# Optimization experiments

Measured on AMD Instinct MI355X. Metric: run time of the kernel, lower is better.

The kernel has to match this reference:

```python
import jax, jax.numpy as jnp
import numpy as np

B, T, NEMBD, HEAD = 8, 2048, 1024, 64

def setup_inputs() -> dict:
    key = jax.random.key(0)
    ks = jax.random.split(key, 6)
    return {
        "values": jax.random.normal(ks[0], (B, T, NEMBD), dtype=jnp.float32),
        "keys": jax.random.normal(ks[1], (B, T, NEMBD), dtype=jnp.float32),
        "queries": jax.random.normal(ks[2], (B, T, NEMBD), dtype=jnp.float32),
        "Wk": jax.random.normal(ks[3], (NEMBD, HEAD), dtype=jnp.float32) * (NEMBD ** -0.5),
        "Wq": jax.random.normal(ks[4], (NEMBD, HEAD), dtype=jnp.float32) * (NEMBD ** -0.5),
        "Wv": jax.random.normal(ks[5], (NEMBD, HEAD), dtype=jnp.float32) * (NEMBD ** -0.5),
    }

def reference(values, keys, queries, Wk, Wq, Wv):
    Bq, Tq, C = queries.shape  # C = nEmbd; original scales by C**-0.5 (NOT headSize)
    k = keys @ Wk              # [B,T,H]
    q = queries @ Wq           # [B,T,H]
    v = values @ Wv            # [B,T,H]
    weight = jnp.einsum('bth,bsh->bts', q, k) * (C ** -0.5)  # [B,T,T]
    causal = jnp.tril(jnp.ones((Tq, Tq), dtype=bool))
    weight = jnp.where(causal, weight, -jnp.inf)
    weight = jax.nn.softmax(weight, axis=-1)
    # dropout = 0.0 (eval): identity
    out = jnp.einsum('bts,bsh->bth', weight, v)  # [B,T,H]
    return out
```

## Files before the change

kernel.cpp:

```cpp
#include <hip/hip_runtime.h>
#include <hip/hip_bf16.h>

typedef __bf16 bf16x8 __attribute__((ext_vector_type(8)));
typedef float f32x4 __attribute__((ext_vector_type(4)));
typedef unsigned short u16x8 __attribute__((ext_vector_type(8)));

#define NB 8
#define NT 2048
#define NC 1024
#define NH 64

__device__ __forceinline__ unsigned short bfbits(float f) {
    return __builtin_bit_cast(unsigned short, (__bf16)f);
}

__device__ __forceinline__ void gl_lds16(const void* g, void* l) {
    __builtin_amdgcn_global_load_lds(
        (const __attribute__((address_space(1))) void*)g,
        (__attribute__((address_space(3))) void*)l, 16, 0, 0);
}
__device__ __forceinline__ void gl_lds16_nt(const void* g, void* l) {
    __builtin_amdgcn_global_load_lds(
        (const __attribute__((address_space(1))) void*)g,
        (__attribute__((address_space(3))) void*)l, 16, 0, 2);
}

__global__ __launch_bounds__(256) void wt_kernel(const float* __restrict__ Wq,
                                                 const float* __restrict__ Wk,
                                                 const float* __restrict__ Wv,
                                                 unsigned short* __restrict__ Wt) {
    int idx = blockIdx.x * 256 + threadIdx.x;
    int n = idx >> 16;
    int r = idx & 65535;
    int c = r >> 6;
    int h = r & 63;
    const float* W = (n == 0) ? Wq : ((n == 1) ? Wk : Wv);
    float x = W[c * 64 + h];
    Wt[(n << 16) + h * 1024 + c] = bfbits(x);
}

__global__ __launch_bounds__(256, 3) void proj_kernel(const float* __restrict__ Xv,
                                                      const float* __restrict__ Xk,
                                                      const float* __restrict__ Xq,
                                                      const unsigned short* __restrict__ Wt,
                                                      unsigned short* __restrict__ Q,
                                                      unsigned short* __restrict__ K,
                                                      unsigned short* __restrict__ VT) {
    __shared__ __align__(16) char Xs[2][16384];
    __shared__ __align__(16) char Ws[2][8192];

    int type = blockIdx.x >> 8;
    int mt   = blockIdx.x & 255;
    int row0 = mt << 6;
    int phase = mt & 15;
    const float* X = (type == 0) ? Xq : ((type == 1) ? Xk : Xv);

    int tid  = threadIdx.x;
    int w    = tid >> 6;
    int lane = tid & 63;
    int lo = lane & 15, hi = lane >> 4;
    int swz = (lo & 7) << 4;

    const char* Xbase = (const char*)X + (size_t)row0 * 4096;
    const char* Wbase = (const char*)(Wt + (type << 16));

    int xr_l = lane >> 4;
    int xc_l = (lane & 15) * 16;
    int wr_l = lane >> 3;
    int wc_l = (lane & 7) * 16;

    f32x4 acc[4];
#pragma unroll
    for (int ct = 0; ct < 4; ++ct) acc[ct] = 0.f;

    auto stage = [&](int kc, int buf) {
#pragma unroll
        for (int i = 0; i < 4; ++i) {
            int g = w * 4 + i;
            int r = g * 4 + xr_l;
            gl_lds16_nt(Xbase + (size_t)r * 4096 + kc * 256 + (xc_l ^ ((r & 7) << 4)),
                        Xs[buf] + g * 1024);
        }
#pragma unroll
        for (int i = 0; i < 2; ++i) {
            int g = w * 2 + i;
            int h = g * 8 + wr_l;
            gl_lds16(Wbase + (size_t)h * 2048 + kc * 128 + (wc_l ^ ((h & 7) << 4)),
                     Ws[buf] + g * 1024);
        }
    };

    auto compute = [&](int buf) {
        const char* xrow = Xs[buf] + (w * 16 + lo) * 256;
        const char* wb   = Ws[buf];
#pragma unroll
        for (int ks = 0; ks < 2; ++ks) {
            f32x4 a0 = *(const f32x4*)(xrow + ((ks * 128 + hi * 32) ^ swz));
            f32x4 a1 = *(const f32x4*)(xrow + ((ks * 128 + hi * 32 + 16) ^ swz));
            bf16x8 af;
            af[0] = (__bf16)a0[0]; af[1] = (__bf16)a0[1]; af[2] = (__bf16)a0[2]; af[3] = (__bf16)a0[3];
            af[4] = (__bf16)a1[0]; af[5] = (__bf16)a1[1]; af[6] = (__bf16)a1[2]; af[7] = (__bf16)a1[3];
#pragma unroll
            for (int ct = 0; ct < 4; ++ct) {
                bf16x8 bf = *(const bf16x8*)(wb + (ct * 16 + lo) * 128 + ((ks * 64 + hi * 16) ^ swz));
                acc[ct] = __builtin_amdgcn_mfma_f32_16x16x32_bf16(af, bf, acc[ct], 0, 0, 0);
            }
        }
    };

    stage(phase, 0);
    stage((1 + phase) & 15, 1);

    for (int c = 0; c < 16; ++c) {
        int buf = c & 1;
        if (c < 15) asm volatile("s_waitcnt vmcnt(6)" ::: "memory");
        else        asm volatile("s_waitcnt vmcnt(0)" ::: "memory");
        __builtin_amdgcn_s_barrier();
        compute(buf);
        if (c + 2 < 16) {
            __builtin_amdgcn_s_barrier();
            stage((c + 2 + phase) & 15, buf);
        }
    }

    if (type < 2) {
        unsigned short* O = (type == 0) ? Q : K;
#pragma unroll
        for (int ct = 0; ct < 4; ++ct)
#pragma unroll
            for (int r = 0; r < 4; ++r) {
                int row = row0 + w * 16 + hi * 4 + r;
                int h = lo + 16 * ct;
                O[(size_t)row * NH + h] = bfbits(acc[ct][r]);
            }
    } else {
        int trow = row0 + w * 16 + hi * 4;
        int b = trow >> 11;
        int t = trow & 2047;
#pragma unroll
        for (int ct = 0; ct < 4; ++ct) {
            int h = lo + 16 * ct;
            ushort4 pk;
            pk.x = bfbits(acc[ct][0]);
            pk.y = bfbits(acc[ct][1]);
            pk.z = bfbits(acc[ct][2]);
            pk.w = bfbits(acc[ct][3]);
            *(ushort4*)(VT + (size_t)(b * NH + h) * NT + t) = pk;
        }
    }
}

__global__ __launch_bounds__(256, 2) void attn_kernel(const unsigned short* __restrict__ Q,
                                                      const unsigned short* __restrict__ K,
                                                      const unsigned short* __restrict__ VT,
                                                      float* __restrict__ out) {
    __shared__ __align__(16) unsigned short p_lds[4 * 1024];
    __shared__ __align__(16) float acc_lds[4 * 16 * 64];
    __shared__ float l_lds[4][16];

    int b = blockIdx.x & 7;
    int j = blockIdx.x >> 3;
    int w    = threadIdx.x >> 6;
    int lane = threadIdx.x & 63;
    int lo = lane & 15, hi = lane >> 4;

    const float SC = 0.03125f * 1.44269504088896340736f;
    unsigned short* pl = p_lds + w * 1024;
    char* plb = (char*)pl;

    for (int t2 = 0; t2 < 2; ++t2) {
        int qt = t2 ? (127 - j) : j;
        int q0 = qt << 4;

        const unsigned short* qb = Q + (size_t)(b * NT + q0 + lo) * NH + hi * 8;
        bf16x8 qr0 = *(const bf16x8*)(qb);
        bf16x8 qr1 = *(const bf16x8*)(qb + 32);
        bf16x8 qf0, qf1;
#pragma unroll
        for (int jj = 0; jj < 8; ++jj) {
            qf0[jj] = (__bf16)((float)qr0[jj] * SC);
            qf1[jj] = (__bf16)((float)qr1[jj] * SC);
        }

        int Ct = (q0 + 79) >> 6;
        int c0 = (Ct * w) >> 2;
        int c1 = (Ct * (w + 1)) >> 2;

        float l[4];
        f32x4 acc[4];
#pragma unroll
        for (int r = 0; r < 4; ++r) l[r] = 0.f;
#pragma unroll
        for (int ct = 0; ct < 4; ++ct) acc[ct] = 0.f;

        bf16x8 kn[8], vn[8];
        if (c0 < c1) {
            const unsigned short* kp = K + (size_t)(b * NT + (c0 << 6) + lo) * NH + hi * 8;
            const unsigned short* vp = VT + (size_t)(b * NH + lo) * NT + (c0 << 6) + hi * 8;
#pragma unroll
            for (int g = 0; g < 4; ++g) {
                kn[2 * g]     = *(const bf16x8*)(kp + g * 16 * NH);
                kn[2 * g + 1] = *(const bf16x8*)(kp + g * 16 * NH + 32);
                vn[2 * g]     = *(const bf16x8*)(vp + g * 16 * NT);
                vn[2 * g + 1] = *(const bf16x8*)(vp + g * 16 * NT + 32);
            }
        }

        for (int c = c0; c < c1; ++c) {
            int s0 = c << 6;
            bf16x8 kk[8], vv[8];
#pragma unroll
            for (int i = 0; i < 8; ++i) { kk[i] = kn[i]; vv[i] = vn[i]; }
            if (c + 1 < c1) {
                const unsigned short* kp2 = K + (size_t)(b * NT + ((c + 1) << 6) + lo) * NH + hi * 8;
                const unsigned short* vp2 = VT + (size_t)(b * NH + lo) * NT + ((c + 1) << 6) + hi * 8;
#pragma unroll
                for (int g = 0; g < 4; ++g) {
                    kn[2 * g]     = *(const bf16x8*)(kp2 + g * 16 * NH);
                    kn[2 * g + 1] = *(const bf16x8*)(kp2 + g * 16 * NH + 32);
                    vn[2 * g]     = *(const bf16x8*)(vp2 + g * 16 * NT);
                    vn[2 * g + 1] = *(const bf16x8*)(vp2 + g * 16 * NT + 32);
                }
            }

            f32x4 S[4];
#pragma unroll
            for (int t = 0; t < 4; ++t) {
                f32x4 s = 0.f;
                s = __builtin_amdgcn_mfma_f32_16x16x32_bf16(qf0, kk[2 * t], s, 0, 0, 0);
                s = __builtin_amdgcn_mfma_f32_16x16x32_bf16(qf1, kk[2 * t + 1], s, 0, 0, 0);
                S[t] = s;
            }

#pragma unroll
            for (int r = 0; r < 4; ++r) {
                int qi = q0 + hi * 4 + r;
                int ql = hi * 4 + r;
                int sw = (ql & 7) << 4;
                float psum = 0.f;
#pragma unroll
                for (int t = 0; t < 4; ++t) {
                    int sk = s0 + t * 16 + lo;
                    float p = (sk <= qi) ? exp2f(S[t][r] - 32.f) : 0.f;
                    psum += p;
                    int byte = ql * 128 + ((((t * 16 + lo) * 2)) ^ sw);
                    *(unsigned short*)(plb + byte) = bfbits(p);
                }
                l[r] += psum;
            }

            int rsw = (lo & 7) << 4;
            bf16x8 pa0 = *(const bf16x8*)(plb + lo * 128 + ((hi * 16) ^ rsw));
            bf16x8 pa1 = *(const bf16x8*)(plb + lo * 128 + (((4 + hi) * 16) ^ rsw));
            acc[0] = __builtin_amdgcn_mfma_f32_16x16x32_bf16(pa0, vv[0], acc[0], 0, 0, 0);
            acc[1] = __builtin_amdgcn_mfma_f32_16x16x32_bf16(pa0, vv[2], acc[1], 0, 0, 0);
            acc[2] = __builtin_amdgcn_mfma_f32_16x16x32_bf16(pa0, vv[4], acc[2], 0, 0, 0);
            acc[3] = __builtin_amdgcn_mfma_f32_16x16x32_bf16(pa0, vv[6], acc[3], 0, 0, 0);
            acc[0] = __builtin_amdgcn_mfma_f32_16x16x32_bf16(pa1, vv[1], acc[0], 0, 0, 0);
            acc[1] = __builtin_amdgcn_mfma_f32_16x16x32_bf16(pa1, vv[3], acc[1], 0, 0, 0);
            acc[2] = __builtin_amdgcn_mfma_f32_16x16x32_bf16(pa1, vv[5], acc[2], 0, 0, 0);
            acc[3] = __builtin_amdgcn_mfma_f32_16x16x32_bf16(pa1, vv[7], acc[3], 0, 0, 0);
        }

#pragma unroll
        for (int d = 1; d < 16; d <<= 1)
#pragma unroll
            for (int r = 0; r < 4; ++r)
                l[r] += __shfl_xor(l[r], d, 16);

#pragma unroll
        for (int r = 0; r < 4; ++r) {
            int ql = hi * 4 + r;
#pragma unroll
            for (int ct = 0; ct < 4; ++ct)
                acc_lds[(w * 16 + ql) * 64 + lo + 16 * ct] = acc[ct][r];
        }
        if (lo == 0) {
#pragma unroll
            for (int r = 0; r < 4; ++r)
                l_lds[w][hi * 4 + r] = l[r];
        }
        __syncthreads();

        int q  = threadIdx.x >> 4;
        int h0 = (threadIdx.x & 15) << 2;
        float L = l_lds[0][q] + l_lds[1][q] + l_lds[2][q] + l_lds[3][q];
        float ox = 0.f, oy = 0.f, oz = 0.f, ow = 0.f;
#pragma unroll
        for (int ww = 0; ww < 4; ++ww) {
            const float* p = acc_lds + (ww * 16 + q) * 64 + h0;
            ox += p[0]; oy += p[1]; oz += p[2]; ow += p[3];
        }
        float inv = 1.0f / L;
        float4 res = make_float4(ox * inv, oy * inv, oz * inv, ow * inv);
        *(float4*)(out + (size_t)(b * NT + q0 + q) * NH + h0) = res;
        __syncthreads();
    }
}

extern "C" void kernel_launch(void* const* d_in, const int* in_sizes, int n_in,
                              void* d_out, int out_size, void* d_ws, size_t ws_size,
                              hipStream_t stream) {
    const float* values  = (const float*)d_in[0];
    const float* keys    = (const float*)d_in[1];
    const float* queries = (const float*)d_in[2];
    const float* Wk = (const float*)d_in[3];
    const float* Wq = (const float*)d_in[4];
    const float* Wv = (const float*)d_in[5];
    float* out = (float*)d_out;

    unsigned short* Wt = (unsigned short*)d_ws;
    unsigned short* Qb = Wt + 196608;
    unsigned short* Kb = Qb + 1048576;
    unsigned short* VT = Kb + 1048576;

    wt_kernel<<<768, 256, 0, stream>>>(Wq, Wk, Wv, Wt);
    proj_kernel<<<768, 256, 0, stream>>>(values, keys, queries, Wt, Qb, Kb, VT);
    attn_kernel<<<512, 256, 0, stream>>>(Qb, Kb, VT, out);
}
```

Measured before the change: 77.41 us.

## Interleave two query tiles per block and load V per chunk directly

Each block now processes its two query tiles (j and 127-j) together, alternating chunks between them, instead of one after the other. Each tile gets its own LDS P buffer, so the independent chains give the scheduler more instruction-level parallelism. V is now loaded at the start of each chunk rather than prefetched a chunk ahead, while K stays prefetched. This raises register pressure and doubles the P LDS footprint, and the V loads are less hidden.

```diff
diff --git a/kernel.cpp b/kernel.cpp
--- a/kernel.cpp
+++ b/kernel.cpp
@@ -150,11 +150,72 @@
     }
 }
 
+#define LOADK(c_, kn_)                                                                   \
+    {                                                                                    \
+        const unsigned short* kp_ = K + (size_t)(b * NT + ((c_) << 6) + lo) * NH + hi * 8; \
+        _Pragma("unroll")                                                                \
+        for (int g = 0; g < 4; ++g) {                                                    \
+            kn_[2 * g]     = *(const bf16x8*)(kp_ + g * 16 * NH);                        \
+            kn_[2 * g + 1] = *(const bf16x8*)(kp_ + g * 16 * NH + 32);                   \
+        }                                                                                \
+    }
+
+#define CHUNK(q0_, c_, c1_, kn_, qf0_, qf1_, acc_, l_, plb_)                             \
+    {                                                                                    \
+        int s0_ = (c_) << 6;                                                             \
+        const unsigned short* vb_ = VT + (size_t)(b * NH + lo) * NT + s0_ + hi * 8;      \
+        bf16x8 v0_ = *(const bf16x8*)(vb_);                                              \
+        bf16x8 v1_ = *(const bf16x8*)(vb_ + 16 * NT);                                    \
+        bf16x8 v2_ = *(const bf16x8*)(vb_ + 32 * NT);                                    \
+        bf16x8 v3_ = *(const bf16x8*)(vb_ + 48 * NT);                                    \
+        bf16x8 v4_ = *(const bf16x8*)(vb_ + 32);                                         \
+        bf16x8 v5_ = *(const bf16x8*)(vb_ + 16 * NT + 32);                               \
+        bf16x8 v6_ = *(const bf16x8*)(vb_ + 32 * NT + 32);                               \
+        bf16x8 v7_ = *(const bf16x8*)(vb_ + 48 * NT + 32);                               \
+        f32x4 S_[4];                                                                     \
+        _Pragma("unroll")                                                                \
+        for (int t = 0; t < 4; ++t) {                                                    \
+            f32x4 s_ = 0.f;                                                              \
+            s_ = __builtin_amdgcn_mfma_f32_16x16x32_bf16(qf0_, kn_[2 * t], s_, 0, 0, 0); \
+            s_ = __builtin_amdgcn_mfma_f32_16x16x32_bf16(qf1_, kn_[2 * t + 1], s_, 0, 0, 0); \
+            S_[t] = s_;                                                                  \
+        }                                                                                \
+        if ((c_) + 1 < (c1_)) LOADK((c_) + 1, kn_);       \
+        _Pragma("unroll")                                                                \
+        for (int r = 0; r < 4; ++r) {                                                    \
+            int qi_ = (q0_) + hi * 4 + r;                                                \
+            int ql_ = hi * 4 + r;                                                        \
+            int sw_ = (ql_ & 7) << 4;                                                    \
+            float ps_ = 0.f;                                                             \
+            _Pragma("unroll")                                                            \
+            for (int t = 0; t < 4; ++t) {                                                \
+                int sk_ = s0_ + t * 16 + lo;                                             \
+                float p_ = (sk_ <= qi_) ? exp2f(S_[t][r] - 32.f) : 0.f;                  \
+                ps_ += p_;                                                               \
+                int byte_ = ql_ * 128 + ((((t * 16 + lo) * 2)) ^ sw_);                   \
+                *(unsigned short*)((plb_) + byte_) = bfbits(p_);                         \
+            }                                                                            \
+            l_[r] += ps_;                                                                \
+        }                                                                                \
+        int rsw_ = (lo & 7) << 4;                                                        \
+        bf16x8 pa0_ = *(const bf16x8*)((plb_) + lo * 128 + ((hi * 16) ^ rsw_));          \
+        bf16x8 pa1_ = *(const bf16x8*)((plb_) + lo * 128 + (((4 + hi) * 16) ^ rsw_));    \
+        acc_[0] = __builtin_amdgcn_mfma_f32_16x16x32_bf16(pa0_, v0_, acc_[0], 0, 0, 0);  \
+        acc_[1] = __builtin_amdgcn_mfma_f32_16x16x32_bf16(pa0_, v1_, acc_[1], 0, 0, 0);  \
+        acc_[2] = __builtin_amdgcn_mfma_f32_16x16x32_bf16(pa0_, v2_, acc_[2], 0, 0, 0);  \
+        acc_[3] = __builtin_amdgcn_mfma_f32_16x16x32_bf16(pa0_, v3_, acc_[3], 0, 0, 0);  \
+        acc_[0] = __builtin_amdgcn_mfma_f32_16x16x32_bf16(pa1_, v4_, acc_[0], 0, 0, 0);  \
+        acc_[1] = __builtin_amdgcn_mfma_f32_16x16x32_bf16(pa1_, v5_, acc_[1], 0, 0, 0);  \
+        acc_[2] = __builtin_amdgcn_mfma_f32_16x16x32_bf16(pa1_, v6_, acc_[2], 0, 0, 0);  \
+        acc_[3] = __builtin_amdgcn_mfma_f32_16x16x32_bf16(pa1_, v7_, acc_[3], 0, 0, 0);  \
+        ++(c_);                                                                          \
+    }
+
 __global__ __launch_bounds__(256, 2) void attn_kernel(const unsigned short* __restrict__ Q,
                                                       const unsigned short* __restrict__ K,
                                                       const unsigned short* __restrict__ VT,
                                                       float* __restrict__ out) {
-    __shared__ __align__(16) unsigned short p_lds[4 * 1024];
+    __shared__ __align__(16) unsigned short p_lds[8 * 1024];
     __shared__ __align__(16) float acc_lds[4 * 16 * 64];
     __shared__ float l_lds[4][16];
 
@@ -165,123 +226,72 @@
     int lo = lane & 15, hi = lane >> 4;
 
     const float SC = 0.03125f * 1.44269504088896340736f;
-    unsigned short* pl = p_lds + w * 1024;
-    char* plb = (char*)pl;
-
-    for (int t2 = 0; t2 < 2; ++t2) {
-        int qt = t2 ? (127 - j) : j;
-        int q0 = qt << 4;
-
-        const unsigned short* qb = Q + (size_t)(b * NT + q0 + lo) * NH + hi * 8;
-        bf16x8 qr0 = *(const bf16x8*)(qb);
-        bf16x8 qr1 = *(const bf16x8*)(qb + 32);
-        bf16x8 qf0, qf1;
+    char* plbA = (char*)p_lds + w * 4096;
+    char* plbB = plbA + 2048;
+
+    int q0A = j << 4;
+    int q0B = (127 - j) << 4;
+
+    bf16x8 qA0, qA1, qB0, qB1;
+    {
+        const unsigned short* qa = Q + (size_t)(b * NT + q0A + lo) * NH + hi * 8;
+        const unsigned short* qb2 = Q + (size_t)(b * NT + q0B + lo) * NH + hi * 8;
+        bf16x8 ra0 = *(const bf16x8*)(qa);
+        bf16x8 ra1 = *(const bf16x8*)(qa + 32);
+        bf16x8 rb0 = *(const bf16x8*)(qb2);
+        bf16x8 rb1 = *(const bf16x8*)(qb2 + 32);
 #pragma unroll
         for (int jj = 0; jj < 8; ++jj) {
-            qf0[jj] = (__bf16)((float)qr0[jj] * SC);
-            qf1[jj] = (__bf16)((float)qr1[jj] * SC);
-        }
-
-        int Ct = (q0 + 79) >> 6;
-        int c0 = (Ct * w) >> 2;
-        int c1 = (Ct * (w + 1)) >> 2;
-
-        float l[4];
-        f32x4 acc[4];
-#pragma unroll
-        for (int r = 0; r < 4; ++r) l[r] = 0.f;
-#pragma unroll
-        for (int ct = 0; ct < 4; ++ct) acc[ct] = 0.f;
-
-        bf16x8 kn[8], vn[8];
-        if (c0 < c1) {
-            const unsigned short* kp = K + (size_t)(b * NT + (c0 << 6) + lo) * NH + hi * 8;
-            const unsigned short* vp = VT + (size_t)(b * NH + lo) * NT + (c0 << 6) + hi * 8;
-#pragma unroll
-            for (int g = 0; g < 4; ++g) {
-                kn[2 * g]     = *(const bf16x8*)(kp + g * 16 * NH);
-                kn[2 * g + 1] = *(const bf16x8*)(kp + g * 16 * NH + 32);
-                vn[2 * g]     = *(const bf16x8*)(vp + g * 16 * NT);
-                vn[2 * g + 1] = *(const bf16x8*)(vp + g * 16 * NT + 32);
-            }
-        }
-
-        for (int c = c0; c < c1; ++c) {
-            int s0 = c << 6;
-            bf16x8 kk[8], vv[8];
-#pragma unroll
-            for (int i = 0; i < 8; ++i) { kk[i] = kn[i]; vv[i] = vn[i]; }
-            if (c + 1 < c1) {
-                const unsigned short* kp2 = K + (size_t)(b * NT + ((c + 1) << 6) + lo) * NH + hi * 8;
-                const unsigned short* vp2 = VT + (size_t)(b * NH + lo) * NT + ((c + 1) << 6) + hi * 8;
-#pragma unroll
-                for (int g = 0; g < 4; ++g) {
-                    kn[2 * g]     = *(const bf16x8*)(kp2 + g * 16 * NH);
-                    kn[2 * g + 1] = *(const bf16x8*)(kp2 + g * 16 * NH + 32);
-                    vn[2 * g]     = *(const bf16x8*)(vp2 + g * 16 * NT);
-                    vn[2 * g + 1] = *(const bf16x8*)(vp2 + g * 16 * NT + 32);
-                }
-            }
-
-            f32x4 S[4];
-#pragma unroll
-            for (int t = 0; t < 4; ++t) {
-                f32x4 s = 0.f;
-                s = __builtin_amdgcn_mfma_f32_16x16x32_bf16(qf0, kk[2 * t], s, 0, 0, 0);
-                s = __builtin_amdgcn_mfma_f32_16x16x32_bf16(qf1, kk[2 * t + 1], s, 0, 0, 0);
-                S[t] = s;
-            }
-
-#pragma unroll
-            for (int r = 0; r < 4; ++r) {
-                int qi = q0 + hi * 4 + r;
-                int ql = hi * 4 + r;
-                int sw = (ql & 7) << 4;
-                float psum = 0.f;
-#pragma unroll
-                for (int t = 0; t < 4; ++t) {
-                    int sk = s0 + t * 16 + lo;
-                    float p = (sk <= qi) ? exp2f(S[t][r] - 32.f) : 0.f;
-                    psum += p;
-                    int byte = ql * 128 + ((((t * 16 + lo) * 2)) ^ sw);
-                    *(unsigned short*)(plb + byte) = bfbits(p);
-                }
-                l[r] += psum;
-            }
-
-            int rsw = (lo & 7) << 4;
-            bf16x8 pa0 = *(const bf16x8*)(plb + lo * 128 + ((hi * 16) ^ rsw));
-            bf16x8 pa1 = *(const bf16x8*)(plb + lo * 128 + (((4 + hi) * 16) ^ rsw));
-            acc[0] = __builtin_amdgcn_mfma_f32_16x16x32_bf16(pa0, vv[0], acc[0], 0, 0, 0);
-            acc[1] = __builtin_amdgcn_mfma_f32_16x16x32_bf16(pa0, vv[2], acc[1], 0, 0, 0);
-            acc[2] = __builtin_amdgcn_mfma_f32_16x16x32_bf16(pa0, vv[4], acc[2], 0, 0, 0);
-            acc[3] = __builtin_amdgcn_mfma_f32_16x16x32_bf16(pa0, vv[6], acc[3], 0, 0, 0);
-            acc[0] = __builtin_amdgcn_mfma_f32_16x16x32_bf16(pa1, vv[1], acc[0], 0, 0, 0);
-            acc[1] = __builtin_amdgcn_mfma_f32_16x16x32_bf16(pa1, vv[3], acc[1], 0, 0, 0);
-            acc[2] = __builtin_amdgcn_mfma_f32_16x16x32_bf16(pa1, vv[5], acc[2], 0, 0, 0);
-            acc[3] = __builtin_amdgcn_mfma_f32_16x16x32_bf16(pa1, vv[7], acc[3], 0, 0, 0);
-        }
-
-#pragma unroll
-        for (int d = 1; d < 16; d <<= 1)
-#pragma unroll
-            for (int r = 0; r < 4; ++r)
-                l[r] += __shfl_xor(l[r], d, 16);
-
+            qA0[jj] = (__bf16)((float)ra0[jj] * SC);
+            qA1[jj] = (__bf16)((float)ra1[jj] * SC);
+            qB0[jj] = (__bf16)((float)rb0[jj] * SC);
+            qB1[jj] = (__bf16)((float)rb1[jj] * SC);
+        }
+    }
+
+    int CtA = (q0A + 79) >> 6;
+    int CtB = (q0B + 79) >> 6;
+    int cA = (CtA * w) >> 2, c1A = (CtA * (w + 1)) >> 2;
+    int cB = (CtB * w) >> 2, c1B = (CtB * (w + 1)) >> 2;
+
+    float lA[4], lB[4];
+    f32x4 accA[4], accB[4];
+#pragma unroll
+    for (int r = 0; r < 4; ++r) { lA[r] = 0.f; lB[r] = 0.f; }
+#pragma unroll
+    for (int ct = 0; ct < 4; ++ct) { accA[ct] = 0.f; accB[ct] = 0.f; }
+
+    bf16x8 knA[8], knB[8];
+    if (cA < c1A) LOADK(cA, knA);
+    if (cB < c1B) LOADK(cB, knB);
+
+    while (cA < c1A || cB < c1B) {
+        if (cA < c1A) CHUNK(q0A, cA, c1A, knA, qA0, qA1, accA, lA, plbA);
+        if (cB < c1B) CHUNK(q0B, cB, c1B, knB, qB0, qB1, accB, lB, plbB);
+    }
+
+#pragma unroll
+    for (int d = 1; d < 16; d <<= 1)
 #pragma unroll
         for (int r = 0; r < 4; ++r) {
-            int ql = hi * 4 + r;
-#pragma unroll
-            for (int ct = 0; ct < 4; ++ct)
-                acc_lds[(w * 16 + ql) * 64 + lo + 16 * ct] = acc[ct][r];
-        }
-        if (lo == 0) {
-#pragma unroll
-            for (int r = 0; r < 4; ++r)
-                l_lds[w][hi * 4 + r] = l[r];
-        }
-        __syncthreads();
-
+            lA[r] += __shfl_xor(lA[r], d, 16);
+            lB[r] += __shfl_xor(lB[r], d, 16);
+        }
+
+#pragma unroll
+    for (int r = 0; r < 4; ++r) {
+        int ql = hi * 4 + r;
+#pragma unroll
+        for (int ct = 0; ct < 4; ++ct)
+            acc_lds[(w * 16 + ql) * 64 + lo + 16 * ct] = accA[ct][r];
+    }
+    if (lo == 0) {
+#pragma unroll
+        for (int r = 0; r < 4; ++r)
+            l_lds[w][hi * 4 + r] = lA[r];
+    }
+    __syncthreads();
+    {
         int q  = threadIdx.x >> 4;
         int h0 = (threadIdx.x & 15) << 2;
         float L = l_lds[0][q] + l_lds[1][q] + l_lds[2][q] + l_lds[3][q];
@@ -292,9 +302,37 @@
             ox += p[0]; oy += p[1]; oz += p[2]; ow += p[3];
         }
         float inv = 1.0f / L;
-        float4 res = make_float4(ox * inv, oy * inv, oz * inv, ow * inv);
-        *(float4*)(out + (size_t)(b * NT + q0 + q) * NH + h0) = res;
-        __syncthreads();
+        *(float4*)(out + (size_t)(b * NT + q0A + q) * NH + h0) =
+            make_float4(ox * inv, oy * inv, oz * inv, ow * inv);
+    }
+    __syncthreads();
+
+#pragma unroll
+    for (int r = 0; r < 4; ++r) {
+        int ql = hi * 4 + r;
+#pragma unroll
+        for (int ct = 0; ct < 4; ++ct)
+            acc_lds[(w * 16 + ql) * 64 + lo + 16 * ct] = accB[ct][r];
+    }
+    if (lo == 0) {
+#pragma unroll
+        for (int r = 0; r < 4; ++r)
+            l_lds[w][hi * 4 + r] = lB[r];
+    }
+    __syncthreads();
+    {
+        int q  = threadIdx.x >> 4;
+        int h0 = (threadIdx.x & 15) << 2;
+        float L = l_lds[0][q] + l_lds[1][q] + l_lds[2][q] + l_lds[3][q];
+        float ox = 0.f, oy = 0.f, oz = 0.f, ow = 0.f;
+#pragma unroll
+        for (int ww = 0; ww < 4; ++ww) {
+            const float* p = acc_lds + (ww * 16 + q) * 64 + h0;
+            ox += p[0]; oy += p[1]; oz += p[2]; ow += p[3];
+        }
+        float inv = 1.0f / L;
+        *(float4*)(out + (size_t)(b * NT + q0B + q) * NH + h0) =
+            make_float4(ox * inv, oy * inv, oz * inv, ow * inv);
     }
 }
 
```

Measured after the change: 76.44 us. Within noise of the previous version (-1.2%).
